# Optimization experiments

Hardware: AMD Instinct MI355X
Metric: run time of the kernel (lower is better)

Reference implementation:

```python
import jax, jax.numpy as jnp
import numpy as np

B, T, C, H = 2, 1024, 1024, 16
HD = C // H  # head_dim = 64


def setup_inputs() -> dict:
    key = jax.random.key(0)
    ks = jax.random.split(key, 11)
    s = 0.02  # init scale for weights
    inp = {
        "Q": jax.random.normal(ks[0], (B, T, C), jnp.float32),
        "K": jax.random.normal(ks[1], (B, T, C), jnp.float32),
        "V": jax.random.normal(ks[2], (B, T, C), jnp.float32),
        "Wq": jax.random.normal(ks[3], (C, C), jnp.float32) * s,
        "bq": jnp.zeros((C,), jnp.float32),
        "Wk": jax.random.normal(ks[4], (C, C), jnp.float32) * s,
        "bk": jnp.zeros((C,), jnp.float32),
        "Wv": jax.random.normal(ks[5], (C, C), jnp.float32) * s,
        "bv": jnp.zeros((C,), jnp.float32),
        "Wp": jax.random.normal(ks[6], (C, C), jnp.float32) * s,
        "bp": jax.random.normal(ks[7], (C,), jnp.float32) * s,
        # causal attention mask: True = masked (matches masked_fill semantics)
        "attn_mask": jnp.triu(jnp.ones((T, T), jnp.bool_), k=1),
    }
    return inp


def reference(Q, K, V, Wq, bq, Wk, bk, Wv, bv, Wp, bp, attn_mask):
    b, t, c = Q.shape

    def proj(x, W, bias):
        # nn.Linear: x @ W.T + b, then split heads -> [B, H, T, HD]
        return (x @ W.T + bias).reshape(b, t, H, HD).transpose(0, 2, 1, 3)

    q = proj(Q, Wq, bq)
    k = proj(K, Wk, bk)
    v = proj(V, Wv, bv)
    # scoreF: scaled dot-product -> [B, H, T, T]
    a = jnp.einsum('bhtd,bhsd->bhts', q, k) / jnp.sqrt(jnp.asarray(HD, q.dtype))
    a = jnp.where(attn_mask, -jnp.inf, a)  # masked_fill(attn_mask, -inf)
    a = jax.nn.softmax(a, axis=-1)  # ADropout is identity (p=0)
    y = jnp.einsum('bhts,bhsd->bhtd', a, v)  # a @ v
    y = y.transpose(0, 2, 1, 3).reshape(b, t, c)
    y = y @ Wp.T + bp  # P projection; RDropout identity (p=0)
    return (y, a)
```

## Files before the change

### kernel.cpp

```cpp
#include <hip/hip_runtime.h>
#include <hip/hip_bf16.h>

typedef short bf16x8 __attribute__((ext_vector_type(8)));
typedef float f32x4 __attribute__((ext_vector_type(4)));
typedef unsigned short u16;
typedef u16 u16x4 __attribute__((ext_vector_type(4)));
typedef u16 u16x8 __attribute__((ext_vector_type(8)));

#define MFMA16(a, b, c) __builtin_amdgcn_mfma_f32_16x16x32_bf16(a, b, c, 0, 0, 0)


__device__ __forceinline__ u16 f2bf(float f) {
    unsigned u = __builtin_bit_cast(unsigned, f);
    unsigned r = (u + 0x7FFFu + ((u >> 16) & 1u)) >> 16;
    return (u16)r;
}

__device__ __forceinline__ float bf2f(u16 v) {
    return __builtin_bit_cast(float, ((unsigned)v) << 16);
}

__global__ __launch_bounds__(256) void cvt_bf16(
    const float* __restrict__ Q, const float* __restrict__ K, const float* __restrict__ V,
    const float* __restrict__ Wq, const float* __restrict__ Wk, const float* __restrict__ Wv,
    const float* __restrict__ Wp,
    u16* __restrict__ Qb, u16* __restrict__ Kb, u16* __restrict__ Vb,
    u16* __restrict__ Wqb, u16* __restrict__ Wkb, u16* __restrict__ Wvb,
    u16* __restrict__ Wpb) {
    const int z = blockIdx.y;
    const float* src;
    u16* dst;
    int n;
    switch (z) {
        case 0: src = Q;  dst = Qb;  n = 1 << 21; break;
        case 1: src = K;  dst = Kb;  n = 1 << 21; break;
        case 2: src = V;  dst = Vb;  n = 1 << 21; break;
        case 3: src = Wq; dst = Wqb; n = 1 << 20; break;
        case 4: src = Wk; dst = Wkb; n = 1 << 20; break;
        case 5: src = Wv; dst = Wvb; n = 1 << 20; break;
        default: src = Wp; dst = Wpb; n = 1 << 20; break;
    }
    const int i = (blockIdx.x * 256 + threadIdx.x) * 8;
    if (i >= n) return;
    float4 f0 = *(const float4*)(src + i);
    float4 f1 = *(const float4*)(src + i + 4);
    u16x8 t;
    t[0] = f2bf(f0.x); t[1] = f2bf(f0.y); t[2] = f2bf(f0.z); t[3] = f2bf(f0.w);
    t[4] = f2bf(f1.x); t[5] = f2bf(f1.y); t[6] = f2bf(f1.z); t[7] = f2bf(f1.w);
    *(u16x8*)(dst + i) = t;
}

template <int BM, int BN, bool OF32>
__device__ inline void gemm_body(const u16* __restrict__ A,
                                 const u16* __restrict__ W,
                                 const float* __restrict__ bias,
                                 void* __restrict__ outp, int mode) {
    __shared__ u16 As[BM * 64];
    __shared__ u16 Bs[BN * 64];

    const int tid = threadIdx.x;
    const int wave = tid >> 6, lane = tid & 63;
    const int quad = lane >> 4, l16 = lane & 15;
    constexpr int WM = BM / 2;
    constexpr int WN = BN / 2;
    constexpr int MI = WM / 16;
    constexpr int NI = WN / 16;
    const int wm = (wave >> 1) * WM;
    const int wn = (wave & 1) * WN;
    const int m0 = blockIdx.y * BM;
    const int n0 = blockIdx.x * BN;

    f32x4 acc[MI][NI] = {};

    const int lrow = lane >> 3;
    const int lseg = lane & 7;
    const u16* Ag = A + (size_t)(m0 + wave * 8 + lrow) * 1024 + lseg * 8;
    const u16* Wg = W + (size_t)(n0 + wave * 8 + lrow) * 1024 + lseg * 8;
    u16* AsBase = As + wave * 8 * 64;
    u16* BsBase = Bs + wave * 8 * 64;

    for (int kt = 0; kt < 16; ++kt) {
        const int k0 = kt * 64;
        __syncthreads();
#pragma unroll
        for (int rr = 0; rr < BM / 32; ++rr)
            __builtin_amdgcn_global_load_lds(
                (const __attribute__((address_space(1))) void*)(Ag + (size_t)rr * 32 * 1024 + k0),
                (__attribute__((address_space(3))) void*)(AsBase + rr * 32 * 64), 16, 0, 0);
#pragma unroll
        for (int rr = 0; rr < BN / 32; ++rr)
            __builtin_amdgcn_global_load_lds(
                (const __attribute__((address_space(1))) void*)(Wg + (size_t)rr * 32 * 1024 + k0),
                (__attribute__((address_space(3))) void*)(BsBase + rr * 32 * 64), 16, 0, 0);
        __syncthreads();
#pragma unroll
        for (int ks = 0; ks < 2; ++ks) {
            bf16x8 af[MI], bfr[NI];
#pragma unroll
            for (int mi = 0; mi < MI; ++mi)
                af[mi] = *(const bf16x8*)(As + (wm + mi * 16 + l16) * 64 + ks * 32 + quad * 8);
#pragma unroll
            for (int ni = 0; ni < NI; ++ni)
                bfr[ni] = *(const bf16x8*)(Bs + (wn + ni * 16 + l16) * 64 + ks * 32 + quad * 8);
#pragma unroll
            for (int mi = 0; mi < MI; ++mi)
#pragma unroll
                for (int ni = 0; ni < NI; ++ni)
                    acc[mi][ni] = MFMA16(af[mi], bfr[ni], acc[mi][ni]);
        }
    }

#pragma unroll
    for (int ni = 0; ni < NI; ++ni) {
        const int n = n0 + wn + ni * 16 + l16;
        const float bv = bias[n];
#pragma unroll
        for (int mi = 0; mi < MI; ++mi) {
#pragma unroll
            for (int r = 0; r < 4; ++r) {
                const int m = m0 + wm + mi * 16 + quad * 4 + r;
                const float val = acc[mi][ni][r] + bv;
                size_t idx;
                if (mode == 0) {
                    int b = m >> 10, t = m & 1023, h = n >> 6, d = n & 63;
                    idx = ((size_t)((b * 16 + h) * 1024 + t)) * 64 + d;
                } else if (mode == 1) {
                    int b = m >> 10, t = m & 1023, h = n >> 6, d = n & 63;
                    idx = ((size_t)((b * 16 + h) * 64 + d)) * 1024 + t;
                } else {
                    idx = (size_t)m * 1024 + n;
                }
                if (OF32) ((float*)outp)[idx] = val;
                else      ((u16*)outp)[idx] = f2bf(val);
            }
        }
    }
}

__global__ __launch_bounds__(256) void proj_qkv(
    const u16* __restrict__ Qb, const u16* __restrict__ Kb, const u16* __restrict__ Vb,
    const u16* __restrict__ Wqb, const u16* __restrict__ Wkb, const u16* __restrict__ Wvb,
    const float* __restrict__ bq, const float* __restrict__ bk, const float* __restrict__ bv,
    u16* __restrict__ q_ws, u16* __restrict__ k_ws, u16* __restrict__ vt_ws) {
    const int z = blockIdx.z;
    const u16* A = (z == 0) ? Qb : (z == 1) ? Kb : Vb;
    const u16* W = (z == 0) ? Wqb : (z == 1) ? Wkb : Wvb;
    const float* bias = (z == 0) ? bq : (z == 1) ? bk : bv;
    u16* out = (z == 0) ? q_ws : (z == 1) ? k_ws : vt_ws;
    gemm_body<128, 128, false>(A, W, bias, out, (z == 2) ? 1 : 0);
}

__global__ __launch_bounds__(256) void proj_out(
    const u16* __restrict__ A, const u16* __restrict__ Wpb,
    const float* __restrict__ bp, float* __restrict__ y) {
    gemm_body<64, 64, true>(A, Wpb, bp, y, 2);
}

__global__ __launch_bounds__(256) void attn_fused(
    const u16* __restrict__ q_ws, const u16* __restrict__ k_ws,
    const u16* __restrict__ vt_ws, float* __restrict__ a_out,
    u16* __restrict__ ao_ws) {
    __shared__ u16 Pall[4][4][1024];
    __shared__ float Ls[4][16];
    __shared__ float Lrl[16];

    const int tid = threadIdx.x;
    const int wave = tid >> 6, lane = tid & 63;
    const int quad = lane >> 4, l16 = lane & 15;

    const int id = blockIdx.x;
    const int wgid = (id & 7) * 256 + (id >> 3);
    const int bh = wgid >> 6;
    const int strip = 63 - (wgid & 63);
    const int b = bh >> 4, h = bh & 15;
    const int wrow = strip * 16;
    const int nt = (strip >> 2) + 1;

    const u16* qh = q_ws + (size_t)bh * 65536;
    const u16* kh = k_ws + (size_t)bh * 65536;
    const u16* vh = vt_ws + (size_t)bh * 65536;
    float* ah = a_out + ((size_t)bh << 20);

    bf16x8 qf[2];
    qf[0] = *(const bf16x8*)(qh + (size_t)(wrow + l16) * 64 + quad * 8);
    qf[1] = *(const bf16x8*)(qh + (size_t)(wrow + l16) * 64 + 32 + quad * 8);

    float sum_r[4] = {0.f, 0.f, 0.f, 0.f};
    f32x4 o[4] = {};

    for (int s = 0; s < 4; ++s) {
        const int ct = wave + s * 4;
        if (ct < nt) {
            f32x4 c[4] = {};
#pragma unroll
            for (int ks = 0; ks < 2; ++ks)
#pragma unroll
                for (int cb = 0; cb < 4; ++cb) {
                    bf16x8 kf = *(const bf16x8*)(kh + (size_t)(ct * 64 + cb * 16 + l16) * 64 + ks * 32 + quad * 8);
                    c[cb] = MFMA16(qf[ks], kf, c[cb]);
                }
#pragma unroll
            for (int cb = 0; cb < 4; ++cb) {
                const int s_col = cb * 16 + l16;
                const int col = ct * 64 + s_col;
#pragma unroll
                for (int r = 0; r < 4; ++r) {
                    const int m = quad * 4 + r;
                    const int trow = wrow + m;
                    float E = __expf(c[cb][r] * 0.125f - 20.0f);
                    if (col > trow) E = 0.0f;
                    sum_r[r] += E;
                    Pall[wave][s][(s_col >> 3) * 128 + m * 8 + (s_col & 7)] = f2bf(E);
                }
            }
#pragma unroll
            for (int ks = 0; ks < 2; ++ks) {
                bf16x8 pf = *(const bf16x8*)(&Pall[wave][s][(ks * 4 + quad) * 128 + l16 * 8]);
#pragma unroll
                for (int nb = 0; nb < 4; ++nb) {
                    bf16x8 vf = *(const bf16x8*)(vh + (size_t)(nb * 16 + l16) * 1024 + ct * 64 + ks * 32 + quad * 8);
                    o[nb] = MFMA16(pf, vf, o[nb]);
                }
            }
        }
    }

    {
        const f32x4 zz = {0.f, 0.f, 0.f, 0.f};
        for (int ct = nt + wave; ct < 16; ct += 4) {
#pragma unroll
            for (int j = 0; j < 4; ++j)
                __builtin_nontemporal_store(
                    zz, (f32x4*)(ah + (size_t)(wrow + j * 4 + quad) * 1024 + ct * 64 + l16 * 4));
        }
    }

#pragma unroll
    for (int r = 0; r < 4; ++r) {
#pragma unroll
        for (int off = 1; off < 16; off <<= 1)
            sum_r[r] += __shfl_xor(sum_r[r], off);
    }
    if (l16 == 0) {
#pragma unroll
        for (int r = 0; r < 4; ++r) Ls[wave][quad * 4 + r] = sum_r[r];
    }
    __syncthreads();

    float rl[4];
#pragma unroll
    for (int r = 0; r < 4; ++r) {
        const int m = quad * 4 + r;
        rl[r] = 1.0f / (Ls[0][m] + Ls[1][m] + Ls[2][m] + Ls[3][m]);
    }
    if (wave == 0 && l16 == 0) {
#pragma unroll
        for (int r = 0; r < 4; ++r) Lrl[quad * 4 + r] = rl[r];
    }
    __syncthreads();

    {
        const int col4 = l16 * 4;
        const int kseg = col4 >> 3, koff = col4 & 7;
        for (int s = 0; s < 4; ++s) {
            const int ct = wave + s * 4;
            if (ct < nt) {
#pragma unroll
                for (int i = 0; i < 4; ++i) {
                    const int row = quad + i * 4;
                    const u16x4 pv = *(const u16x4*)(&Pall[wave][s][kseg * 128 + row * 8 + koff]);
                    const float rlr = Lrl[row];
                    f32x4 vv;
                    vv[0] = bf2f(pv[0]) * rlr;
                    vv[1] = bf2f(pv[1]) * rlr;
                    vv[2] = bf2f(pv[2]) * rlr;
                    vv[3] = bf2f(pv[3]) * rlr;
                    __builtin_nontemporal_store(
                        vv, (f32x4*)(ah + (size_t)(wrow + row) * 1024 + ct * 64 + col4));
                }
            }
        }
    }

    float* Osum_w = (float*)&Pall[wave][0][0];
#pragma unroll
    for (int nb = 0; nb < 4; ++nb)
#pragma unroll
        for (int r = 0; r < 4; ++r) {
            const int row = quad * 4 + r;
            const int d = nb * 16 + l16;
            Osum_w[row * 64 + (d ^ ((row >> 2) << 4))] = o[nb][r] * rl[r];
        }
    __syncthreads();

#pragma unroll
    for (int i = 0; i < 4; ++i) {
        const int e = tid + i * 256;
        const int row = e >> 6, d = e & 63;
        const int sd = row * 64 + (d ^ ((row >> 2) << 4));
        float v = 0.f;
#pragma unroll
        for (int w = 0; w < 4; ++w)
            v += ((const float*)&Pall[w][0][0])[sd];
        ao_ws[((size_t)(b * 1024 + wrow + row)) * 1024 + h * 64 + d] = f2bf(v);
    }
}

extern "C" void kernel_launch(void* const* d_in, const int* in_sizes, int n_in,
                              void* d_out, int out_size, void* d_ws, size_t ws_size,
                              hipStream_t stream) {
    const float* Q  = (const float*)d_in[0];
    const float* K  = (const float*)d_in[1];
    const float* V  = (const float*)d_in[2];
    const float* Wq = (const float*)d_in[3];
    const float* bq = (const float*)d_in[4];
    const float* Wk = (const float*)d_in[5];
    const float* bk = (const float*)d_in[6];
    const float* Wv = (const float*)d_in[7];
    const float* bv = (const float*)d_in[8];
    const float* Wp = (const float*)d_in[9];
    const float* bp = (const float*)d_in[10];

    float* y = (float*)d_out;
    float* a = y + (size_t)2 * 1024 * 1024;

    const size_t M1 = (size_t)1 << 20;
    u16* q_ws  = (u16*)d_ws;
    u16* k_ws  = q_ws  + 2 * M1;
    u16* vt_ws = k_ws  + 2 * M1;
    u16* ao_ws = vt_ws + 2 * M1;
    u16* Qb    = ao_ws + 2 * M1;
    u16* Kb    = Qb    + 2 * M1;
    u16* Vb    = Kb    + 2 * M1;
    u16* Wqb   = Vb    + 2 * M1;
    u16* Wkb   = Wqb   + M1;
    u16* Wvb   = Wkb   + M1;
    u16* Wpb   = Wvb   + M1;

    hipLaunchKernelGGL(cvt_bf16, dim3(1024, 7), dim3(256), 0, stream,
                       Q, K, V, Wq, Wk, Wv, Wp, Qb, Kb, Vb, Wqb, Wkb, Wvb, Wpb);
    hipLaunchKernelGGL(proj_qkv, dim3(8, 16, 3), dim3(256), 0, stream,
                       Qb, Kb, Vb, Wqb, Wkb, Wvb, bq, bk, bv, q_ws, k_ws, vt_ws);
    hipLaunchKernelGGL(attn_fused, dim3(2048), dim3(256), 0, stream,
                       q_ws, k_ws, vt_ws, a, ao_ws);
    hipLaunchKernelGGL(proj_out, dim3(16, 32, 1), dim3(256), 0, stream,
                       ao_ws, Wpb, bp, y);
}
```

Before: 264.6 us.

## Keep attention scores in registers via transposed MFMA and shrink QKV projection tiles

Result: no change. 261.8 us (-1.1%).

```diff
diff --git a/kernel.cpp b/kernel.cpp
--- a/kernel.cpp
+++ b/kernel.cpp
@@ -14,10 +14,6 @@
     unsigned u = __builtin_bit_cast(unsigned, f);
     unsigned r = (u + 0x7FFFu + ((u >> 16) & 1u)) >> 16;
     return (u16)r;
-}
-
-__device__ __forceinline__ float bf2f(u16 v) {
-    return __builtin_bit_cast(float, ((unsigned)v) << 16);
 }
 
 __global__ __launch_bounds__(256) void cvt_bf16(
@@ -147,7 +143,7 @@
     const u16* W = (z == 0) ? Wqb : (z == 1) ? Wkb : Wvb;
     const float* bias = (z == 0) ? bq : (z == 1) ? bk : bv;
     u16* out = (z == 0) ? q_ws : (z == 1) ? k_ws : vt_ws;
-    gemm_body<128, 128, false>(A, W, bias, out, (z == 2) ? 1 : 0);
+    gemm_body<128, 64, false>(A, W, bias, out, (z == 2) ? 1 : 0);
 }
 
 __global__ __launch_bounds__(256) void proj_out(
@@ -160,9 +156,10 @@
     const u16* __restrict__ q_ws, const u16* __restrict__ k_ws,
     const u16* __restrict__ vt_ws, float* __restrict__ a_out,
     u16* __restrict__ ao_ws) {
-    __shared__ u16 Pall[4][4][1024];
+    __shared__ u16 P[4][1024];
     __shared__ float Ls[4][16];
     __shared__ float Lrl[16];
+    __shared__ float Osum[4][1024];
 
     const int tid = threadIdx.x;
     const int wave = tid >> 6, lane = tid & 63;
@@ -185,37 +182,80 @@
     qf[0] = *(const bf16x8*)(qh + (size_t)(wrow + l16) * 64 + quad * 8);
     qf[1] = *(const bf16x8*)(qh + (size_t)(wrow + l16) * 64 + 32 + quad * 8);
 
-    float sum_r[4] = {0.f, 0.f, 0.f, 0.f};
-    f32x4 o[4] = {};
-
+    const int qrow = wrow + l16;
+    const int swz = (l16 & 7) << 4;
+
+    f32x4 c[4][4] = {};
+    float sum_l = 0.f;
+
+#pragma unroll
     for (int s = 0; s < 4; ++s) {
         const int ct = wave + s * 4;
         if (ct < nt) {
-            f32x4 c[4] = {};
 #pragma unroll
             for (int ks = 0; ks < 2; ++ks)
 #pragma unroll
                 for (int cb = 0; cb < 4; ++cb) {
                     bf16x8 kf = *(const bf16x8*)(kh + (size_t)(ct * 64 + cb * 16 + l16) * 64 + ks * 32 + quad * 8);
-                    c[cb] = MFMA16(qf[ks], kf, c[cb]);
+                    c[s][cb] = MFMA16(kf, qf[ks], c[s][cb]);
                 }
 #pragma unroll
             for (int cb = 0; cb < 4; ++cb) {
-                const int s_col = cb * 16 + l16;
-                const int col = ct * 64 + s_col;
 #pragma unroll
                 for (int r = 0; r < 4; ++r) {
-                    const int m = quad * 4 + r;
-                    const int trow = wrow + m;
-                    float E = __expf(c[cb][r] * 0.125f - 20.0f);
-                    if (col > trow) E = 0.0f;
-                    sum_r[r] += E;
-                    Pall[wave][s][(s_col >> 3) * 128 + m * 8 + (s_col & 7)] = f2bf(E);
+                    const int kg = ct * 64 + cb * 16 + quad * 4 + r;
+                    float E = __expf(c[s][cb][r] * 0.125f - 20.0f);
+                    if (kg > qrow) E = 0.0f;
+                    c[s][cb][r] = E;
+                    sum_l += E;
                 }
             }
+        }
+    }
+
+    {
+        const f32x4 zz = {0.f, 0.f, 0.f, 0.f};
+        for (int ct = nt + wave; ct < 16; ct += 4) {
+#pragma unroll
+            for (int j = 0; j < 4; ++j)
+                __builtin_nontemporal_store(
+                    zz, (f32x4*)(ah + (size_t)(wrow + j * 4 + quad) * 1024 + ct * 64 + l16 * 4));
+        }
+    }
+
+    sum_l += __shfl_xor(sum_l, 16);
+    sum_l += __shfl_xor(sum_l, 32);
+    if (lane < 16) Ls[wave][lane] = sum_l;
+    __syncthreads();
+    if (wave == 0 && lane < 16)
+        Lrl[lane] = 1.0f / (Ls[0][lane] + Ls[1][lane] + Ls[2][lane] + Ls[3][lane]);
+    __syncthreads();
+
+    const float rl_me = Lrl[l16];
+
+    u16* Pw = &P[wave][0];
+    f32x4 o[4] = {};
+#pragma unroll
+    for (int s = 0; s < 4; ++s) {
+        const int ct = wave + s * 4;
+        if (ct < nt) {
+#pragma unroll
+            for (int cb = 0; cb < 4; ++cb) {
+                f32x4 vv;
+                u16x4 pk;
+#pragma unroll
+                for (int r = 0; r < 4; ++r) {
+                    const float v = c[s][cb][r] * rl_me;
+                    vv[r] = v;
+                    pk[r] = f2bf(v);
+                }
+                __builtin_nontemporal_store(
+                    vv, (f32x4*)(ah + (size_t)qrow * 1024 + ct * 64 + cb * 16 + quad * 4));
+                *(u16x4*)((char*)Pw + ((l16 * 128 + cb * 32 + quad * 8) ^ swz)) = pk;
+            }
 #pragma unroll
             for (int ks = 0; ks < 2; ++ks) {
-                bf16x8 pf = *(const bf16x8*)(&Pall[wave][s][(ks * 4 + quad) * 128 + l16 * 8]);
+                bf16x8 pf = *(const bf16x8*)((const char*)Pw + ((l16 * 128 + (ks * 4 + quad) * 16) ^ swz));
 #pragma unroll
                 for (int nb = 0; nb < 4; ++nb) {
                     bf16x8 vf = *(const bf16x8*)(vh + (size_t)(nb * 16 + l16) * 1024 + ct * 64 + ks * 32 + quad * 8);
@@ -225,71 +265,13 @@
         }
     }
 
-    {
-        const f32x4 zz = {0.f, 0.f, 0.f, 0.f};
-        for (int ct = nt + wave; ct < 16; ct += 4) {
-#pragma unroll
-            for (int j = 0; j < 4; ++j)
-                __builtin_nontemporal_store(
-                    zz, (f32x4*)(ah + (size_t)(wrow + j * 4 + quad) * 1024 + ct * 64 + l16 * 4));
-        }
-    }
-
-#pragma unroll
-    for (int r = 0; r < 4; ++r) {
-#pragma unroll
-        for (int off = 1; off < 16; off <<= 1)
-            sum_r[r] += __shfl_xor(sum_r[r], off);
-    }
-    if (l16 == 0) {
-#pragma unroll
-        for (int r = 0; r < 4; ++r) Ls[wave][quad * 4 + r] = sum_r[r];
-    }
-    __syncthreads();
-
-    float rl[4];
-#pragma unroll
-    for (int r = 0; r < 4; ++r) {
-        const int m = quad * 4 + r;
-        rl[r] = 1.0f / (Ls[0][m] + Ls[1][m] + Ls[2][m] + Ls[3][m]);
-    }
-    if (wave == 0 && l16 == 0) {
-#pragma unroll
-        for (int r = 0; r < 4; ++r) Lrl[quad * 4 + r] = rl[r];
-    }
-    __syncthreads();
-
-    {
-        const int col4 = l16 * 4;
-        const int kseg = col4 >> 3, koff = col4 & 7;
-        for (int s = 0; s < 4; ++s) {
-            const int ct = wave + s * 4;
-            if (ct < nt) {
-#pragma unroll
-                for (int i = 0; i < 4; ++i) {
-                    const int row = quad + i * 4;
-                    const u16x4 pv = *(const u16x4*)(&Pall[wave][s][kseg * 128 + row * 8 + koff]);
-                    const float rlr = Lrl[row];
-                    f32x4 vv;
-                    vv[0] = bf2f(pv[0]) * rlr;
-                    vv[1] = bf2f(pv[1]) * rlr;
-                    vv[2] = bf2f(pv[2]) * rlr;
-                    vv[3] = bf2f(pv[3]) * rlr;
-                    __builtin_nontemporal_store(
-                        vv, (f32x4*)(ah + (size_t)(wrow + row) * 1024 + ct * 64 + col4));
-                }
-            }
-        }
-    }
-
-    float* Osum_w = (float*)&Pall[wave][0][0];
 #pragma unroll
     for (int nb = 0; nb < 4; ++nb)
 #pragma unroll
         for (int r = 0; r < 4; ++r) {
             const int row = quad * 4 + r;
             const int d = nb * 16 + l16;
-            Osum_w[row * 64 + (d ^ ((row >> 2) << 4))] = o[nb][r] * rl[r];
+            Osum[wave][row * 64 + (d ^ ((row >> 2) << 4))] = o[nb][r];
         }
     __syncthreads();
 
@@ -298,10 +280,7 @@
         const int e = tid + i * 256;
         const int row = e >> 6, d = e & 63;
         const int sd = row * 64 + (d ^ ((row >> 2) << 4));
-        float v = 0.f;
-#pragma unroll
-        for (int w = 0; w < 4; ++w)
-            v += ((const float*)&Pall[w][0][0])[sd];
+        const float v = Osum[0][sd] + Osum[1][sd] + Osum[2][sd] + Osum[3][sd];
         ao_ws[((size_t)(b * 1024 + wrow + row)) * 1024 + h * 64 + d] = f2bf(v);
     }
 }
@@ -339,7 +318,7 @@
 
     hipLaunchKernelGGL(cvt_bf16, dim3(1024, 7), dim3(256), 0, stream,
                        Q, K, V, Wq, Wk, Wv, Wp, Qb, Kb, Vb, Wqb, Wkb, Wvb, Wpb);
-    hipLaunchKernelGGL(proj_qkv, dim3(8, 16, 3), dim3(256), 0, stream,
+    hipLaunchKernelGGL(proj_qkv, dim3(16, 16, 3), dim3(256), 0, stream,
                        Qb, Kb, Vb, Wqb, Wkb, Wvb, bq, bk, bv, q_ws, k_ws, vt_ws);
     hipLaunchKernelGGL(attn_fused, dim3(2048), dim3(256), 0, stream,
                        q_ws, k_ws, vt_ws, a, ao_ws);
```
